# Optimization experiments

Hardware: AMD Instinct MI355X
Metric: run time of the kernel (lower is better)

Reference implementation:

```python
import jax, jax.numpy as jnp
import numpy as np

B, T, D = 32, 2048, 1024


def setup_inputs() -> dict:
    key = jax.random.key(0)
    k1, k2, k3, k4, k5, k6 = jax.random.split(key, 6)
    return {
        "keys": jax.random.normal(k1, (B, T, D), dtype=jnp.float32),
        "value": jax.random.normal(k2, (B, T, D), dtype=jnp.float32),
        "query": jax.random.normal(k3, (B, D), dtype=jnp.float32),
        "weight_feedback": jax.random.normal(k4, (B, T, D), dtype=jnp.float32),
        "v": jax.random.normal(k5, (D,), dtype=jnp.float32) / np.sqrt(D),
        "enc_seq_len": jax.random.randint(k6, (B,), 1, T + 1, dtype=jnp.int32),
    }


def reference(keys, value, query, weight_feedback, v, enc_seq_len):
    # energies = v^T tanh(key + query + weight_feedback)  -> [B, T]
    hidden = jnp.tanh(keys + query[:, None, :] + weight_feedback)  # [B,T,D]
    energies = jnp.einsum("btd,d->bt", hidden, v)                  # [B,T]
    # length mask + softmax over time
    mask = jnp.arange(energies.shape[1])[None, :] < enc_seq_len[:, None]  # [B,T]
    energies = jnp.where(mask, energies, -jnp.inf)
    weights = jax.nn.softmax(energies, axis=1)                      # [B,T]
    # context = weights^T value -> [B, D_v]
    context = jnp.einsum("bt,btd->bd", weights, value)
    return context, weights[:, :, None]
```

## Files before the change

kernel.cpp:

```cpp
#include <hip/hip_runtime.h>
#include <math.h>

#define BB 32
#define TT 2048
#define DD 1024
#define TCHUNK 64

__device__ __forceinline__ float fast_tanh(float x) {
    float e = __expf(2.0f * x);
    return 1.0f - __fdividef(2.0f, e + 1.0f);
}

__global__ __launch_bounds__(256) void energies_kernel(
    const float* __restrict__ keys, const float* __restrict__ query,
    const float* __restrict__ wf, const float* __restrict__ v,
    const int* __restrict__ lenp, float* __restrict__ eout)
{
    const int b    = blockIdx.y;
    const int wave = threadIdx.x >> 6;
    const int lane = threadIdx.x & 63;
    const int t    = blockIdx.x * 4 + wave;
    if (t >= lenp[b]) return;

    const size_t row  = ((size_t)b * TT + t) * DD;
    const size_t qrow = (size_t)b * DD;

    float s = 0.0f;
    #pragma unroll
    for (int k = 0; k < 4; k++) {
        const int d = k * 256 + lane * 4;
        const float4 k4 = *(const float4*)(keys + row + d);
        const float4 w4 = *(const float4*)(wf   + row + d);
        const float4 q4 = *(const float4*)(query + qrow + d);
        const float4 v4 = *(const float4*)(v + d);
        s += fast_tanh(k4.x + q4.x + w4.x) * v4.x
           + fast_tanh(k4.y + q4.y + w4.y) * v4.y
           + fast_tanh(k4.z + q4.z + w4.z) * v4.z
           + fast_tanh(k4.w + q4.w + w4.w) * v4.w;
    }
    #pragma unroll
    for (int off = 32; off > 0; off >>= 1) s += __shfl_down(s, off, 64);
    if (lane == 0) eout[(size_t)b * TT + t] = s;
}

__global__ __launch_bounds__(256) void softmax_kernel(
    const int* __restrict__ lenp, float* __restrict__ wrow_all,
    float* __restrict__ context)
{
    const int b = blockIdx.x;
    const int L = lenp[b];
    float* wrow = wrow_all + (size_t)b * TT;

    #pragma unroll
    for (int i = 0; i < 4; i++)
        context[(size_t)b * DD + threadIdx.x + i * 256] = 0.0f;

    float e[8];
    float m = -INFINITY;
    #pragma unroll
    for (int i = 0; i < 8; i++) {
        const int t = threadIdx.x + i * 256;
        e[i] = (t < L) ? wrow[t] : -INFINITY;
        m = fmaxf(m, e[i]);
    }
    #pragma unroll
    for (int off = 1; off < 64; off <<= 1) m = fmaxf(m, __shfl_xor(m, off, 64));
    __shared__ float redm[4];
    const int wv = threadIdx.x >> 6;
    if ((threadIdx.x & 63) == 0) redm[wv] = m;
    __syncthreads();
    m = fmaxf(fmaxf(redm[0], redm[1]), fmaxf(redm[2], redm[3]));

    float s = 0.0f;
    #pragma unroll
    for (int i = 0; i < 8; i++) {
        e[i] = (e[i] == -INFINITY) ? 0.0f : __expf(e[i] - m);
        s += e[i];
    }
    #pragma unroll
    for (int off = 1; off < 64; off <<= 1) s += __shfl_xor(s, off, 64);
    __shared__ float reds[4];
    if ((threadIdx.x & 63) == 0) reds[wv] = s;
    __syncthreads();
    s = reds[0] + reds[1] + reds[2] + reds[3];
    const float inv = 1.0f / s;

    #pragma unroll
    for (int i = 0; i < 8; i++)
        wrow[threadIdx.x + i * 256] = e[i] * inv;
}

__global__ __launch_bounds__(256) void context_kernel(
    const float* __restrict__ value, const float* __restrict__ weights,
    const int* __restrict__ lenp, float* __restrict__ context)
{
    const int b = blockIdx.y;
    const int L = lenp[b];
    const int t0 = blockIdx.x * TCHUNK;
    if (t0 >= L) return;
    const int tend = min(t0 + TCHUNK, L);
    const int d = threadIdx.x * 4;

    __shared__ float wsh[TCHUNK];
    if (threadIdx.x < TCHUNK)
        wsh[threadIdx.x] = weights[(size_t)b * TT + t0 + threadIdx.x];
    __syncthreads();

    float4 acc = make_float4(0.f, 0.f, 0.f, 0.f);
    #pragma unroll 2
    for (int t = t0; t < tend; t++) {
        const float w = wsh[t - t0];
        const float4 v4 = *(const float4*)(value + ((size_t)b * TT + t) * DD + d);
        acc.x += w * v4.x; acc.y += w * v4.y;
        acc.z += w * v4.z; acc.w += w * v4.w;
    }
    float* dst = context + (size_t)b * DD + d;
    atomicAdd(dst + 0, acc.x);
    atomicAdd(dst + 1, acc.y);
    atomicAdd(dst + 2, acc.z);
    atomicAdd(dst + 3, acc.w);
}

extern "C" void kernel_launch(void* const* d_in, const int* in_sizes, int n_in,
                              void* d_out, int out_size, void* d_ws, size_t ws_size,
                              hipStream_t stream) {
    const float* keys  = (const float*)d_in[0];
    const float* value = (const float*)d_in[1];
    const float* query = (const float*)d_in[2];
    const float* wf    = (const float*)d_in[3];
    const float* v     = (const float*)d_in[4];
    const int*   lenp  = (const int*)d_in[5];

    float* out      = (float*)d_out;
    float* context  = out;
    float* weights  = out + BB * DD;

    energies_kernel<<<dim3(TT / 4, BB), 256, 0, stream>>>(keys, query, wf, v, lenp, weights);
    softmax_kernel<<<BB, 256, 0, stream>>>(lenp, weights, context);
    context_kernel<<<dim3(TT / TCHUNK, BB), 256, 0, stream>>>(value, weights, lenp, context);
}
```

Baseline: 596.6 us.

## Fuse softmax into context kernel by recomputing row stats per block

Removes the separate single-block-per-batch softmax launch. Each context block now recomputes the row max and sum from raw energies held in workspace, then normalises its own chunk of weights and accumulates context. Context zeroing moves into the energies kernel. This saves a launch and a serial low-occupancy kernel, at the cost of every block re-reading the full energy row.

```diff
diff --git a/kernel.cpp b/kernel.cpp
--- a/kernel.cpp
+++ b/kernel.cpp
@@ -14,12 +14,18 @@
 __global__ __launch_bounds__(256) void energies_kernel(
     const float* __restrict__ keys, const float* __restrict__ query,
     const float* __restrict__ wf, const float* __restrict__ v,
-    const int* __restrict__ lenp, float* __restrict__ eout)
+    const int* __restrict__ lenp, float* __restrict__ eraw,
+    float* __restrict__ context)
 {
     const int b    = blockIdx.y;
     const int wave = threadIdx.x >> 6;
     const int lane = threadIdx.x & 63;
     const int t    = blockIdx.x * 4 + wave;
+
+    if (blockIdx.x == 0) {
+        *(float4*)(context + (size_t)b * DD + threadIdx.x * 4) =
+            make_float4(0.f, 0.f, 0.f, 0.f);
+    }
     if (t >= lenp[b]) return;
 
     const size_t row  = ((size_t)b * TT + t) * DD;
@@ -40,72 +46,66 @@
     }
     #pragma unroll
     for (int off = 32; off > 0; off >>= 1) s += __shfl_down(s, off, 64);
-    if (lane == 0) eout[(size_t)b * TT + t] = s;
+    if (lane == 0) eraw[(size_t)b * TT + t] = s;
 }
 
-__global__ __launch_bounds__(256) void softmax_kernel(
-    const int* __restrict__ lenp, float* __restrict__ wrow_all,
+__global__ __launch_bounds__(256) void ctx_softmax_kernel(
+    const float* __restrict__ value, const float* __restrict__ eraw,
+    const int* __restrict__ lenp, float* __restrict__ weights,
     float* __restrict__ context)
 {
-    const int b = blockIdx.x;
-    const int L = lenp[b];
-    float* wrow = wrow_all + (size_t)b * TT;
+    const int b  = blockIdx.y;
+    const int L  = lenp[b];
+    const int t0 = blockIdx.x * TCHUNK;
+    float* wrow = weights + (size_t)b * TT;
 
-    #pragma unroll
-    for (int i = 0; i < 4; i++)
-        context[(size_t)b * DD + threadIdx.x + i * 256] = 0.0f;
+    if (t0 >= L) {
+        if (threadIdx.x < TCHUNK) wrow[t0 + threadIdx.x] = 0.0f;
+        return;
+    }
 
-    float e[8];
+    const float* erow = eraw + (size_t)b * TT;
+    const int wv   = threadIdx.x >> 6;
+    const int lane = threadIdx.x & 63;
+
     float m = -INFINITY;
     #pragma unroll
     for (int i = 0; i < 8; i++) {
         const int t = threadIdx.x + i * 256;
-        e[i] = (t < L) ? wrow[t] : -INFINITY;
-        m = fmaxf(m, e[i]);
+        if (t < L) m = fmaxf(m, erow[t]);
     }
     #pragma unroll
     for (int off = 1; off < 64; off <<= 1) m = fmaxf(m, __shfl_xor(m, off, 64));
     __shared__ float redm[4];
-    const int wv = threadIdx.x >> 6;
-    if ((threadIdx.x & 63) == 0) redm[wv] = m;
+    if (lane == 0) redm[wv] = m;
     __syncthreads();
     m = fmaxf(fmaxf(redm[0], redm[1]), fmaxf(redm[2], redm[3]));
 
     float s = 0.0f;
     #pragma unroll
     for (int i = 0; i < 8; i++) {
-        e[i] = (e[i] == -INFINITY) ? 0.0f : __expf(e[i] - m);
-        s += e[i];
+        const int t = threadIdx.x + i * 256;
+        if (t < L) s += __expf(erow[t] - m);
     }
     #pragma unroll
     for (int off = 1; off < 64; off <<= 1) s += __shfl_xor(s, off, 64);
     __shared__ float reds[4];
-    if ((threadIdx.x & 63) == 0) reds[wv] = s;
+    if (lane == 0) reds[wv] = s;
     __syncthreads();
     s = reds[0] + reds[1] + reds[2] + reds[3];
     const float inv = 1.0f / s;
 
-    #pragma unroll
-    for (int i = 0; i < 8; i++)
-        wrow[threadIdx.x + i * 256] = e[i] * inv;
-}
+    __shared__ float wsh[TCHUNK];
+    if (threadIdx.x < TCHUNK) {
+        const int t = t0 + threadIdx.x;
+        const float w = (t < L) ? __expf(erow[t] - m) * inv : 0.0f;
+        wsh[threadIdx.x] = w;
+        wrow[t] = w;
+    }
+    __syncthreads();
 
-__global__ __launch_bounds__(256) void context_kernel(
-    const float* __restrict__ value, const float* __restrict__ weights,
-    const int* __restrict__ lenp, float* __restrict__ context)
-{
-    const int b = blockIdx.y;
-    const int L = lenp[b];
-    const int t0 = blockIdx.x * TCHUNK;
-    if (t0 >= L) return;
     const int tend = min(t0 + TCHUNK, L);
     const int d = threadIdx.x * 4;
-
-    __shared__ float wsh[TCHUNK];
-    if (threadIdx.x < TCHUNK)
-        wsh[threadIdx.x] = weights[(size_t)b * TT + t0 + threadIdx.x];
-    __syncthreads();
-
     float4 acc = make_float4(0.f, 0.f, 0.f, 0.f);
     #pragma unroll 2
     for (int t = t0; t < tend; t++) {
@@ -134,8 +134,10 @@
     float* out      = (float*)d_out;
     float* context  = out;
     float* weights  = out + BB * DD;
+    float* eraw     = (float*)d_ws;
 
-    energies_kernel<<<dim3(TT / 4, BB), 256, 0, stream>>>(keys, query, wf, v, lenp, weights);
-    softmax_kernel<<<BB, 256, 0, stream>>>(lenp, weights, context);
-    context_kernel<<<dim3(TT / TCHUNK, BB), 256, 0, stream>>>(value, weights, lenp, context);
+    energies_kernel<<<dim3(TT / 4, BB), 256, 0, stream>>>(
+        keys, query, wf, v, lenp, eraw, context);
+    ctx_softmax_kernel<<<dim3(TT / TCHUNK, BB), 256, 0, stream>>>(
+        value, eraw, lenp, weights, context);
 }
```

Measured after the change: 597.4 us. No clear change (+0.1%).
